# Optimization experiments

Hardware: AMD Instinct MI355X
Metric: run time of the kernel (lower is better)

The kernel has to match this reference:

```python
import jax, jax.numpy as jnp
import numpy as np

B, N_ATOM, N_TOK = 1, 1536, 384
C_ATOM, C_PAIR, C_TOK = 128, 16, 384
C_HID, H, L = 32, 4, 3
HID = 2 * C_ATOM  # n_transition = 2
N_QUERY, N_KEY, INF = 32, 128, 1e9


def _ln(x, gamma=None, beta=None, eps=1e-5):
    mu = jnp.mean(x, axis=-1, keepdims=True)
    var = jnp.mean(jnp.square(x - mu), axis=-1, keepdims=True)
    y = (x - mu) * jax.lax.rsqrt(var + eps)
    if gamma is not None:
        y = y * gamma
    if beta is not None:
        y = y + beta
    return y


def _adaln(a, s, gamma_s, Wg, bg, Ws):
    an = _ln(a)            # LN without affine
    sn = _ln(s, gamma_s)   # scale-only LN
    return jax.nn.sigmoid(sn @ Wg + bg) * an + sn @ Ws


def _block_mask():
    # AtomTransformer.forward: 32-query x 128-key block-local mask
    offset = N_QUERY // 2 - 0.5
    n_center = N_ATOM // N_QUERY + 1
    centers = offset + jnp.arange(n_center, dtype=jnp.float32) * N_QUERY
    idx = jnp.arange(N_ATOM, dtype=jnp.float32)[:, None]
    row = (jnp.abs(idx - centers[None, :]) < N_QUERY / 2).astype(jnp.float32)
    col = (jnp.abs(idx - centers[None, :]) < N_KEY / 2).astype(jnp.float32)
    return (row @ col.T - 1.0) * INF   # [N,N]: 0 in-window, -INF outside


def _forward(ref_pos, ref_mask, ref_element, ref_charge, ref_atom_name_chars,
             ref_space_uid, token_mask, atom_to_token_index,
             W_feats, W_ref_offset, W_inv_sq, W_valid, W_l, W_m,
             W_mlp1, W_mlp2, W_mlp3, W_out_tok,
             attn_ada_gamma_s, attn_ada_Wg, attn_ada_bg, attn_ada_Ws,
             Wq, bq, Wk, Wv, lnz_g, lnz_b, Wb, Wgate, Wo, Wsg, bsg,
             tr_ada_gamma_s, tr_ada_Wg, tr_ada_bg, tr_ada_Ws,
             tr_W1, tr_W2, tr_Wog, tr_bog, tr_Wout):
    # --- RefAtomFeatureEmbedder (AF3 Alg 5 lines 1-6) ---
    feats = jnp.concatenate([
        ref_pos, ref_mask[..., None], ref_element, ref_charge[..., None],
        ref_atom_name_chars.reshape(B, N_ATOM, -1), ref_space_uid[..., None]], axis=-1)
    cl = feats @ W_feats                                     # [B,N,C_ATOM]
    d = ref_pos[:, None, :, :] - ref_pos[:, :, None, :]      # d[l,m] = pos[m]-pos[l]
    v = (ref_space_uid[:, None, :] == ref_space_uid[:, :, None]).astype(jnp.float32)[..., None]
    plm = (d @ W_ref_offset) * v
    inv_sq = 1.0 / (1.0 + jnp.sum(d * d, axis=-1, keepdims=True))
    plm = plm + (inv_sq @ W_inv_sq) * v + (v @ W_valid) * v  # [B,N,N,C_PAIR]
    ql = cl
    # --- single -> pair conditioning + pair MLP ---
    crelu = jax.nn.relu(cl)
    plm = plm + (crelu @ W_l)[:, :, None, :] + (crelu @ W_m)[:, None, :, :]
    h = jax.nn.relu(plm) @ W_mlp1
    h = jax.nn.relu(h) @ W_mlp2
    h = jax.nn.relu(h) @ W_mlp3
    plm = plm + h
    # --- AtomTransformer (Alg 7) -> DiffusionTransformer (Alg 23) ---
    beta = _block_mask()                                     # [N,N]
    atom_mask = jnp.einsum('blt,bt->bl', atom_to_token_index, token_mask)
    mask_bias = (atom_mask - 1.0)[:, None, None, :] * INF    # [B,1,1,N]
    a, s = ql, cl
    inv_sqrt = 1.0 / np.sqrt(C_HID)
    for i in range(L):
        # AttentionPairBias (Alg 24)
        an = _adaln(a, s, attn_ada_gamma_s[i], attn_ada_Wg[i], attn_ada_bg[i], attn_ada_Ws[i])
        q = (an @ Wq[i] + bq[i]).reshape(B, N_ATOM, H, C_HID)
        k = (an @ Wk[i]).reshape(B, N_ATOM, H, C_HID)
        vv = (an @ Wv[i]).reshape(B, N_ATOM, H, C_HID)
        zb = _ln(plm, lnz_g[i], lnz_b[i]) @ Wb[i]            # [B,N,N,H]
        logits = (jnp.einsum('bqhc,bkhc->bhqk', q, k) * inv_sqrt
                  + jnp.moveaxis(zb, -1, 1) + beta[None, None] + mask_bias)
        A = jax.nn.softmax(logits, axis=-1)
        o = jnp.einsum('bhqk,bkhc->bqhc', A, vv)
        g = jax.nn.sigmoid(an @ Wgate[i]).reshape(B, N_ATOM, H, C_HID)
        o = (g * o).reshape(B, N_ATOM, H * C_HID) @ Wo[i]
        attn_out = jax.nn.sigmoid(s @ Wsg[i] + bsg[i]) * o
        # ConditionedTransitionBlock (Alg 25) on pre-attention a (Alg 23)
        tn = _adaln(a, s, tr_ada_gamma_s[i], tr_ada_Wg[i], tr_ada_bg[i], tr_ada_Ws[i])
        hh = jax.nn.silu(tn @ tr_W1[i]) * (tn @ tr_W2[i])
        tr_out = jax.nn.sigmoid(s @ tr_Wog[i] + tr_bog[i]) * (hh @ tr_Wout[i])
        a = attn_out + tr_out
    # --- mean-aggregate atoms -> tokens (Alg 5 line 15) ---
    al = jax.nn.relu(a @ W_out_tok)                          # [B,N,C_TOK]
    counts = jnp.maximum(jnp.sum(atom_to_token_index, axis=1), 1.0)
    a_tok = jnp.einsum('blt,blc->btc', atom_to_token_index, al) / counts[..., None]
    return a_tok


def setup_inputs() -> dict:
    key = jax.random.key(0)
    ks = iter(jax.random.split(key, 80))

    def nrm(shape, scale=0.02):
        return jax.random.normal(next(ks), shape, dtype=jnp.float32) * scale

    inp = {}
    inp['ref_pos'] = jax.random.normal(next(ks), (B, N_ATOM, 3), dtype=jnp.float32) * 3.0
    inp['ref_mask'] = jnp.ones((B, N_ATOM), jnp.float32)
    elem = jax.random.randint(next(ks), (B, N_ATOM), 0, 128)
    inp['ref_element'] = jax.nn.one_hot(elem, 128, dtype=jnp.float32)
    inp['ref_charge'] = jax.random.normal(next(ks), (B, N_ATOM), dtype=jnp.float32)
    chars = jax.random.randint(next(ks), (B, N_ATOM, 4), 0, 64)
    inp['ref_atom_name_chars'] = jax.nn.one_hot(chars, 64, dtype=jnp.float32)
    inp['ref_space_uid'] = jnp.broadcast_to(
        (jnp.arange(N_ATOM) // 8).astype(jnp.float32), (B, N_ATOM))
    inp['token_mask'] = jnp.ones((B, N_TOK), jnp.float32)
    tok = (jnp.arange(N_ATOM) * N_TOK) // N_ATOM  # ~4 atoms per token
    inp['atom_to_token_index'] = jnp.broadcast_to(
        jax.nn.one_hot(tok, N_TOK, dtype=jnp.float32), (B, N_ATOM, N_TOK))
    # embedder params
    inp['W_feats'] = nrm((390, C_ATOM))
    inp['W_ref_offset'] = nrm((3, C_PAIR))
    inp['W_inv_sq'] = nrm((1, C_PAIR))
    inp['W_valid'] = nrm((1, C_PAIR))
    inp['W_l'] = nrm((C_ATOM, C_PAIR))
    inp['W_m'] = nrm((C_ATOM, C_PAIR))
    inp['W_mlp1'] = nrm((C_PAIR, C_PAIR))
    inp['W_mlp2'] = nrm((C_PAIR, C_PAIR))
    inp['W_mlp3'] = nrm((C_PAIR, C_PAIR))
    inp['W_out_tok'] = nrm((C_ATOM, C_TOK))
    # DiffusionTransformer params, stacked over L blocks
    inp['attn_ada_gamma_s'] = jnp.ones((L, C_ATOM), jnp.float32)
    inp['attn_ada_Wg'] = nrm((L, C_ATOM, C_ATOM))
    inp['attn_ada_bg'] = jnp.zeros((L, C_ATOM), jnp.float32)
    inp['attn_ada_Ws'] = nrm((L, C_ATOM, C_ATOM))
    inp['Wq'] = nrm((L, C_ATOM, H * C_HID))
    inp['bq'] = jnp.zeros((L, H * C_HID), jnp.float32)
    inp['Wk'] = nrm((L, C_ATOM, H * C_HID))
    inp['Wv'] = nrm((L, C_ATOM, H * C_HID))
    inp['lnz_g'] = jnp.ones((L, C_PAIR), jnp.float32)
    inp['lnz_b'] = jnp.zeros((L, C_PAIR), jnp.float32)
    inp['Wb'] = nrm((L, C_PAIR, H))
    inp['Wgate'] = nrm((L, C_ATOM, H * C_HID))
    inp['Wo'] = nrm((L, H * C_HID, C_ATOM))
    inp['Wsg'] = nrm((L, C_ATOM, C_ATOM))
    inp['bsg'] = jnp.full((L, C_ATOM), -2.0, jnp.float32)
    inp['tr_ada_gamma_s'] = jnp.ones((L, C_ATOM), jnp.float32)
    inp['tr_ada_Wg'] = nrm((L, C_ATOM, C_ATOM))
    inp['tr_ada_bg'] = jnp.zeros((L, C_ATOM), jnp.float32)
    inp['tr_ada_Ws'] = nrm((L, C_ATOM, C_ATOM))
    inp['tr_W1'] = nrm((L, C_ATOM, HID))
    inp['tr_W2'] = nrm((L, C_ATOM, HID))
    inp['tr_Wog'] = nrm((L, C_ATOM, C_ATOM))
    inp['tr_bog'] = jnp.full((L, C_ATOM), -2.0, jnp.float32)
    inp['tr_Wout'] = nrm((L, HID, C_ATOM))
    return inp


def reference(ref_pos, ref_mask, ref_element, ref_charge, ref_atom_name_chars,
              ref_space_uid, token_mask, atom_to_token_index,
              W_feats, W_ref_offset, W_inv_sq, W_valid, W_l, W_m,
              W_mlp1, W_mlp2, W_mlp3, W_out_tok,
              attn_ada_gamma_s, attn_ada_Wg, attn_ada_bg, attn_ada_Ws,
              Wq, bq, Wk, Wv, lnz_g, lnz_b, Wb, Wgate, Wo, Wsg, bsg,
              tr_ada_gamma_s, tr_ada_Wg, tr_ada_bg, tr_ada_Ws,
              tr_W1, tr_W2, tr_Wog, tr_bog, tr_Wout):
    return _forward(ref_pos, ref_mask, ref_element, ref_charge, ref_atom_name_chars,
                    ref_space_uid, token_mask, atom_to_token_index,
                    W_feats, W_ref_offset, W_inv_sq, W_valid, W_l, W_m,
                    W_mlp1, W_mlp2, W_mlp3, W_out_tok,
                    attn_ada_gamma_s, attn_ada_Wg, attn_ada_bg, attn_ada_Ws,
                    Wq, bq, Wk, Wv, lnz_g, lnz_b, Wb, Wgate, Wo, Wsg, bsg,
                    tr_ada_gamma_s, tr_ada_Wg, tr_ada_bg, tr_ada_Ws,
                    tr_W1, tr_W2, tr_Wog, tr_bog, tr_Wout)
```

## Files before the change

kernel.cpp:

```cpp
#include <hip/hip_runtime.h>
#include <math.h>

#define N_ATOM 1536
#define NLAYER 3
#define NC     196608L
#define ZSTRIDE 786432L

struct GD { const float* A; const float* B; float* C; const float* ks; const float* bias;
            const float* sg; const float* ad; int act; int ldb; int ldc; int mode; };
struct GB { GD g[18]; };

__global__ __launch_bounds__(128) void embed_tok_kernel(
    const float* __restrict__ pos, const float* __restrict__ rmask,
    const float* __restrict__ elem, const float* __restrict__ charge,
    const float* __restrict__ chars, const float* __restrict__ uid,
    const float* __restrict__ Wf, const float* __restrict__ W_l, const float* __restrict__ W_m,
    const float* __restrict__ a2t, const float* __restrict__ tmask,
    float* __restrict__ cl, float* __restrict__ aa,
    float* __restrict__ pl, float* __restrict__ pm,
    int* __restrict__ tok, float* __restrict__ amask)
{
  int l = blockIdx.x, c = threadIdx.x;
  __shared__ int sidx[6];
  __shared__ float crow[128];
  if (elem[(long)l * 128 + c] > 0.5f) sidx[0] = c;
  float v0 = chars[(long)l * 256 + c];
  if (v0 > 0.5f) sidx[1 + (c >> 6)] = c & 63;
  float v1 = chars[(long)l * 256 + 128 + c];
  if (v1 > 0.5f) sidx[3 + (c >> 6)] = c & 63;
  for (int j = c; j < 384; j += 128)
    if (a2t[(long)l * 384 + j] > 0.5f) sidx[5] = j;
  __syncthreads();
  float acc = pos[l * 3 + 0] * Wf[c]
            + pos[l * 3 + 1] * Wf[128 + c]
            + pos[l * 3 + 2] * Wf[256 + c]
            + rmask[l] * Wf[384 + c]
            + Wf[(4 + sidx[0]) * 128 + c]
            + charge[l] * Wf[132 * 128 + c]
            + Wf[(133 + sidx[1]) * 128 + c]
            + Wf[(197 + sidx[2]) * 128 + c]
            + Wf[(261 + sidx[3]) * 128 + c]
            + Wf[(325 + sidx[4]) * 128 + c]
            + uid[l] * Wf[389 * 128 + c];
  long gi = (long)l * 128 + c;
  cl[gi] = acc; aa[gi] = acc; crow[c] = fmaxf(acc, 0.f);
  __syncthreads();
  if (c < 32) {
    const float* W = (c < 16) ? W_l : W_m;
    int o = c & 15;
    float s = 0.f;
    for (int cc = 0; cc < 128; cc++) s = fmaf(crow[cc], W[cc * 16 + o], s);
    if (c < 16) pl[l * 16 + o] = s; else pm[l * 16 + o] = s;
  }
  if (c == 127) {
    int j = sidx[5];
    tok[l] = j; amask[l] = tmask[j];
  }
}

__device__ __forceinline__ void gemm32_body(float* sm, const GD d, int row0, int col0) {
  float* As = sm;
  float* Bs = sm + 1152;
  float* rmu = sm + 3328;
  float* rsd = sm + 3360;
  int tid = threadIdx.x;
  if (d.mode >= 1) {
    int r = tid >> 3, sgi = tid & 7;
    const float* Ar = d.A + (long)(row0 + r) * 128 + sgi * 16;
    float4 vv[4];
    float s1 = 0.f;
#pragma unroll
    for (int c4 = 0; c4 < 4; c4++) {
      vv[c4] = *(const float4*)(Ar + c4 * 4);
      s1 += vv[c4].x + vv[c4].y + vv[c4].z + vv[c4].w;
    }
    s1 += __shfl_xor(s1, 1); s1 += __shfl_xor(s1, 2); s1 += __shfl_xor(s1, 4);
    float mu = s1 * (1.f / 128.f);
    float s2 = 0.f;
#pragma unroll
    for (int c4 = 0; c4 < 4; c4++) {
      float dx = vv[c4].x - mu, dy = vv[c4].y - mu, dz = vv[c4].z - mu, dw = vv[c4].w - mu;
      s2 += dx * dx + dy * dy + dz * dz + dw * dw;
    }
    s2 += __shfl_xor(s2, 1); s2 += __shfl_xor(s2, 2); s2 += __shfl_xor(s2, 4);
    if (sgi == 0) {
      rmu[r] = mu;
      rsd[r] = rsqrtf(s2 * (1.f / 128.f) + 1e-5f);
    }
  }
  int tx = tid & 15, ty = tid >> 4;
  float acc[2][4] = {};
  for (int k0 = 0; k0 < 128; k0 += 32) {
    __syncthreads();
    { int r = tid >> 3, k4 = tid & 7;
      long gro = (long)(row0 + r) * 128 + k0 + k4 * 4;
      float4 v = *(const float4*)(d.A + gro);
      float vals[4] = {v.x, v.y, v.z, v.w};
      if (d.mode >= 1) {
        float mu = rmu[r], sd = rsd[r];
        if (d.mode == 2) {
          float4 sg4 = *(const float4*)(d.sg + gro);
          float4 ad4 = *(const float4*)(d.ad + gro);
          vals[0] = fmaf(sg4.x, (vals[0] - mu) * sd, ad4.x);
          vals[1] = fmaf(sg4.y, (vals[1] - mu) * sd, ad4.y);
          vals[2] = fmaf(sg4.z, (vals[2] - mu) * sd, ad4.z);
          vals[3] = fmaf(sg4.w, (vals[3] - mu) * sd, ad4.w);
        } else {
#pragma unroll
          for (int cc = 0; cc < 4; cc++) vals[cc] = (vals[cc] - mu) * sd;
        }
      }
      if (d.ks) {
        const float* kp = d.ks + k0 + k4 * 4;
#pragma unroll
        for (int cc = 0; cc < 4; cc++) vals[cc] *= kp[cc];
      }
      As[(k4 * 4 + 0) * 36 + r] = vals[0]; As[(k4 * 4 + 1) * 36 + r] = vals[1];
      As[(k4 * 4 + 2) * 36 + r] = vals[2]; As[(k4 * 4 + 3) * 36 + r] = vals[3];
    }
    for (int e = tid; e < 512; e += 256) {
      int k = e >> 4, n4 = e & 15;
      *(float4*)&Bs[k * 68 + n4 * 4] = *(const float4*)(d.B + (long)(k0 + k) * d.ldb + col0 + n4 * 4);
    }
    __syncthreads();
#pragma unroll
    for (int kk = 0; kk < 32; kk++) {
      float a0 = As[kk * 36 + ty * 2], a1 = As[kk * 36 + ty * 2 + 1];
      float4 b = *(const float4*)&Bs[kk * 68 + tx * 4];
      float bv[4] = {b.x, b.y, b.z, b.w};
#pragma unroll
      for (int j = 0; j < 4; j++) {
        acc[0][j] = fmaf(a0, bv[j], acc[0][j]);
        acc[1][j] = fmaf(a1, bv[j], acc[1][j]);
      }
    }
  }
#pragma unroll
  for (int i = 0; i < 2; i++) {
    int row = row0 + ty * 2 + i;
#pragma unroll
    for (int j = 0; j < 4; j++) {
      int col = col0 + tx * 4 + j;
      float x = acc[i][j];
      if (d.bias) x += d.bias[col];
      if (d.act == 1) x = 1.f / (1.f + expf(-x));
      else if (d.act == 2) x = fmaxf(x, 0.f);
      d.C[(long)row * d.ldc + col] = x;
    }
  }
}

__device__ __forceinline__ void gemm32k64_body(float* sm, const GD d, int row0, int col0) {
  float* As = sm;
  float* Bs = sm + 2304;
  float* rmu = sm + 6656;
  float* rsd = sm + 6688;
  int tid = threadIdx.x;
  if (d.mode >= 1) {
    int r = tid >> 3, sgi = tid & 7;
    const float* Ar = d.A + (long)(row0 + r) * 128 + sgi * 16;
    float4 vv[4];
    float s1 = 0.f;
#pragma unroll
    for (int c4 = 0; c4 < 4; c4++) {
      vv[c4] = *(const float4*)(Ar + c4 * 4);
      s1 += vv[c4].x + vv[c4].y + vv[c4].z + vv[c4].w;
    }
    s1 += __shfl_xor(s1, 1); s1 += __shfl_xor(s1, 2); s1 += __shfl_xor(s1, 4);
    float mu = s1 * (1.f / 128.f);
    float s2 = 0.f;
#pragma unroll
    for (int c4 = 0; c4 < 4; c4++) {
      float dx = vv[c4].x - mu, dy = vv[c4].y - mu, dz = vv[c4].z - mu, dw = vv[c4].w - mu;
      s2 += dx * dx + dy * dy + dz * dz + dw * dw;
    }
    s2 += __shfl_xor(s2, 1); s2 += __shfl_xor(s2, 2); s2 += __shfl_xor(s2, 4);
    if (sgi == 0) {
      rmu[r] = mu;
      rsd[r] = rsqrtf(s2 * (1.f / 128.f) + 1e-5f);
    }
  }
  int tx = tid & 15, ty = tid >> 4;
  float acc[2][4] = {};
  for (int k0 = 0; k0 < 128; k0 += 64) {
    __syncthreads();
    { int r = tid >> 3, k4b = tid & 7;
#pragma unroll
      for (int kh = 0; kh < 2; kh++) {
        int k4 = k4b + kh * 8;
        long gro = (long)(row0 + r) * 128 + k0 + k4 * 4;
        float4 v = *(const float4*)(d.A + gro);
        float vals[4] = {v.x, v.y, v.z, v.w};
        if (d.mode >= 1) {
          float mu = rmu[r], sd = rsd[r];
          if (d.mode == 2) {
            float4 sg4 = *(const float4*)(d.sg + gro);
            float4 ad4 = *(const float4*)(d.ad + gro);
            vals[0] = fmaf(sg4.x, (vals[0] - mu) * sd, ad4.x);
            vals[1] = fmaf(sg4.y, (vals[1] - mu) * sd, ad4.y);
            vals[2] = fmaf(sg4.z, (vals[2] - mu) * sd, ad4.z);
            vals[3] = fmaf(sg4.w, (vals[3] - mu) * sd, ad4.w);
          } else {
#pragma unroll
            for (int cc = 0; cc < 4; cc++) vals[cc] = (vals[cc] - mu) * sd;
          }
        }
        if (d.ks) {
          const float* kp = d.ks + k0 + k4 * 4;
#pragma unroll
          for (int cc = 0; cc < 4; cc++) vals[cc] *= kp[cc];
        }
        As[(k4 * 4 + 0) * 36 + r] = vals[0]; As[(k4 * 4 + 1) * 36 + r] = vals[1];
        As[(k4 * 4 + 2) * 36 + r] = vals[2]; As[(k4 * 4 + 3) * 36 + r] = vals[3];
      } }
    for (int e = tid; e < 1024; e += 256) {
      int k = e >> 4, n4 = e & 15;
      *(float4*)&Bs[k * 68 + n4 * 4] = *(const float4*)(d.B + (long)(k0 + k) * d.ldb + col0 + n4 * 4);
    }
    __syncthreads();
#pragma unroll
    for (int kk = 0; kk < 64; kk++) {
      float a0 = As[kk * 36 + ty * 2], a1 = As[kk * 36 + ty * 2 + 1];
      float4 b = *(const float4*)&Bs[kk * 68 + tx * 4];
      float bv[4] = {b.x, b.y, b.z, b.w};
#pragma unroll
      for (int j = 0; j < 4; j++) {
        acc[0][j] = fmaf(a0, bv[j], acc[0][j]);
        acc[1][j] = fmaf(a1, bv[j], acc[1][j]);
      }
    }
  }
#pragma unroll
  for (int i = 0; i < 2; i++) {
    int row = row0 + ty * 2 + i;
#pragma unroll
    for (int j = 0; j < 4; j++) {
      int col = col0 + tx * 4 + j;
      float x = acc[i][j];
      if (d.bias) x += d.bias[col];
      if (d.act == 1) x = 1.f / (1.f + expf(-x));
      else if (d.act == 2) x = fmaxf(x, 0.f);
      d.C[(long)row * d.ldc + col] = x;
    }
  }
}

__global__ __launch_bounds__(256) void gemm32(GB args)
{
  __shared__ __align__(16) float sm[6720];
  gemm32k64_body(sm, args.g[blockIdx.z], blockIdx.y * 32, blockIdx.x * 64);
}

__global__ __launch_bounds__(256) void zpre_kernel(
    const float* __restrict__ pos, const float* __restrict__ uid,
    const float* __restrict__ Wro, const float* __restrict__ Winv, const float* __restrict__ Wval,
    const float* __restrict__ M1, const float* __restrict__ M2, const float* __restrict__ M3,
    const float* __restrict__ Lg, const float* __restrict__ Lb, const float* __restrict__ Wb,
    const float* __restrict__ pl, const float* __restrict__ pm, float* __restrict__ zb,
    GB ba)
{
  __shared__ __align__(16) float sm[3392];
  int bid = blockIdx.x, tid = threadIdx.x;
  if (bid < 1728) {
    GD d = ba.g[bid / 96];
    int tt = bid % 96;
    gemm32_body(sm, d, (tt >> 1) * 32, (tt & 1) * 64);
    return;
  }
  int zbid = bid - 1728;
  if (tid < 48)  sm[tid] = Wro[tid];
  if (tid < 16)  { sm[48 + tid] = Winv[tid]; sm[64 + tid] = Wval[tid]; }
  sm[80 + tid] = M1[tid]; sm[336 + tid] = M2[tid]; sm[592 + tid] = M3[tid];
  if (tid < 48)  { sm[848 + tid] = Lg[tid]; sm[896 + tid] = Lb[tid]; }
  if (tid < 192) sm[944 + tid] = Wb[tid];
  __syncthreads();
  const float* sWro = sm;      const float* sWinv = sm + 48;  const float* sWval = sm + 64;
  const float* sM1 = sm + 80;  const float* sM2 = sm + 336;   const float* sM3 = sm + 592;
  const float* sLg = sm + 848; const float* sLb = sm + 896;   const float* sWb = sm + 944;
  int b = zbid >> 4;
  int pc = (zbid & 15) * 256 + tid;
  int qi = pc >> 7, kj = pc & 127;
  int l = b * 32 + qi, m = b * 32 - 48 + kj;
  long base = (long)(b * 32 + qi) * 128 + kj;
  if (m < 0 || m >= N_ATOM) {
    for (int i = 0; i < NLAYER; i++)
      for (int h = 0; h < 4; h++) zb[i * ZSTRIDE + h * NC + base] = 0.f;
    return;
  }
  float dx = pos[m * 3 + 0] - pos[l * 3 + 0];
  float dy = pos[m * 3 + 1] - pos[l * 3 + 1];
  float dz = pos[m * 3 + 2] - pos[l * 3 + 2];
  float v = (uid[m] == uid[l]) ? 1.f : 0.f;
  float inv = 1.f / (1.f + dx * dx + dy * dy + dz * dz);
  float pv[16], ha[16], hb[16];
#pragma unroll
  for (int j = 0; j < 16; j++)
    pv[j] = v * (dx * sWro[j] + dy * sWro[16 + j] + dz * sWro[32 + j] + inv * sWinv[j] + sWval[j])
            + pl[l * 16 + j] + pm[m * 16 + j];
#pragma unroll
  for (int jo = 0; jo < 16; jo++) { float s = 0.f; for (int ji = 0; ji < 16; ji++) s = fmaf(fmaxf(pv[ji], 0.f), sM1[ji * 16 + jo], s); ha[jo] = s; }
#pragma unroll
  for (int jo = 0; jo < 16; jo++) { float s = 0.f; for (int ji = 0; ji < 16; ji++) s = fmaf(fmaxf(ha[ji], 0.f), sM2[ji * 16 + jo], s); hb[jo] = s; }
#pragma unroll
  for (int jo = 0; jo < 16; jo++) { float s = 0.f; for (int ji = 0; ji < 16; ji++) s = fmaf(fmaxf(hb[ji], 0.f), sM3[ji * 16 + jo], s); ha[jo] = s; }
#pragma unroll
  for (int j = 0; j < 16; j++) pv[j] += ha[j];
  for (int i = 0; i < NLAYER; i++) {
    float mu = 0.f;
#pragma unroll
    for (int j = 0; j < 16; j++) mu += pv[j];
    mu *= (1.f / 16.f);
    float var = 0.f;
#pragma unroll
    for (int j = 0; j < 16; j++) { float dd = pv[j] - mu; var += dd * dd; }
    var *= (1.f / 16.f);
    float rs = rsqrtf(var + 1e-5f);
    float zn[16];
#pragma unroll
    for (int j = 0; j < 16; j++) zn[j] = (pv[j] - mu) * rs * sLg[i * 16 + j] + sLb[i * 16 + j];
    for (int h = 0; h < 4; h++) {
      float s = 0.f;
#pragma unroll
      for (int j = 0; j < 16; j++) s = fmaf(zn[j], sWb[i * 64 + j * 4 + h], s);
      zb[i * ZSTRIDE + h * NC + base] = s;
    }
  }
}

__global__ __launch_bounds__(256) void attn_tr_kernel(
    const float* __restrict__ qb, const float* __restrict__ kb, const float* __restrict__ vb,
    const float* __restrict__ gb, const float* __restrict__ zb, const float* __restrict__ amask,
    float* __restrict__ go,
    const float* __restrict__ h1, const float* __restrict__ h2, const float* __restrict__ B2,
    const float* __restrict__ g2, float* __restrict__ trbuf)
{
  __shared__ __align__(16) float sm[11904];
  int bid = blockIdx.x, t = threadIdx.x;
  if (bid < 96) {
    int u = bid;
    int row0 = (u >> 1) * 32, col0 = (u & 1) * 64;
    float* As = sm; float* Bs = sm + 2304;
    int tx = t & 15, ty = t >> 4;
    float acc2[2][4] = {};
    for (int k0 = 0; k0 < 256; k0 += 64) {
      __syncthreads();
      { int r = t >> 3, k4b = t & 7;
#pragma unroll
        for (int kh = 0; kh < 2; kh++) {
          int k4 = k4b + kh * 8;
          long o = (long)(row0 + r) * 256 + k0 + k4 * 4;
          float4 x = *(const float4*)(h1 + o);
          float4 y = *(const float4*)(h2 + o);
          As[(k4 * 4 + 0) * 36 + r] = (x.x / (1.f + expf(-x.x))) * y.x;
          As[(k4 * 4 + 1) * 36 + r] = (x.y / (1.f + expf(-x.y))) * y.y;
          As[(k4 * 4 + 2) * 36 + r] = (x.z / (1.f + expf(-x.z))) * y.z;
          As[(k4 * 4 + 3) * 36 + r] = (x.w / (1.f + expf(-x.w))) * y.w;
        } }
      for (int e = t; e < 1024; e += 256) {
        int k = e >> 4, n4 = e & 15;
        *(float4*)&Bs[k * 68 + n4 * 4] = *(const float4*)(B2 + (long)(k0 + k) * 128 + col0 + n4 * 4);
      }
      __syncthreads();
#pragma unroll
      for (int kk = 0; kk < 64; kk++) {
        float a0 = As[kk * 36 + ty * 2], a1 = As[kk * 36 + ty * 2 + 1];
        float4 b = *(const float4*)&Bs[kk * 68 + tx * 4];
        float bv[4] = {b.x, b.y, b.z, b.w};
#pragma unroll
        for (int j = 0; j < 4; j++) {
          acc2[0][j] = fmaf(a0, bv[j], acc2[0][j]);
          acc2[1][j] = fmaf(a1, bv[j], acc2[1][j]);
        }
      }
    }
#pragma unroll
    for (int i = 0; i < 2; i++) {
      long o = (long)(row0 + ty * 2 + i) * 128 + col0 + tx * 4;
      float4 g4 = *(const float4*)(g2 + o);
      float4 r;
      r.x = g4.x * acc2[i][0]; r.y = g4.y * acc2[i][1];
      r.z = g4.z * acc2[i][2]; r.w = g4.w * acc2[i][3];
      *(float4*)(trbuf + o) = r;
    }
    return;
  }
  float* qs = sm;
  float* ks = sm + 576;
  float* vs = sm + 5184;
  float* ps = sm + 9792;
  int u = bid - 96;
  int h = u / 96, bx = u - h * 96;
  int b = bx >> 1, half = bx & 1;
  int q0 = b * 32 + half * 16;
  int kbase = b * 32 - 48;
  const float* zbh = zb + (long)h * NC;
  if (t < 128) {
    int qi = t >> 3, c4 = t & 7;
    *(float4*)&qs[qi * 36 + c4 * 4] = *(const float4*)(qb + (long)(q0 + qi) * 128 + h * 32 + c4 * 4);
  }
  for (int idx = t; idx < 128 * 8; idx += 256) {
    int kj = idx >> 3, c4 = idx & 7;
    int m = kbase + kj;
    float4 kv = make_float4(0.f, 0.f, 0.f, 0.f), vv = make_float4(0.f, 0.f, 0.f, 0.f);
    if (m >= 0 && m < N_ATOM) {
      kv = *(const float4*)(kb + (long)m * 128 + h * 32 + c4 * 4);
      vv = *(const float4*)(vb + (long)m * 128 + h * 32 + c4 * 4);
    }
    *(float4*)&ks[kj * 36 + c4 * 4] = kv;
    *(float4*)&vs[kj * 36 + c4 * 4] = vv;
  }
  __syncthreads();
  const float isq = 0.17677669529663687f;
  for (int p = t; p < 2048; p += 256) {
    int qi = p >> 7, kj = p & 127;
    int m = kbase + kj;
    float s = 0.f;
#pragma unroll
    for (int c4 = 0; c4 < 8; c4++) {
      float4 a = *(const float4*)&qs[qi * 36 + c4 * 4];
      float4 k4 = *(const float4*)&ks[kj * 36 + c4 * 4];
      s = fmaf(a.x, k4.x, s); s = fmaf(a.y, k4.y, s);
      s = fmaf(a.z, k4.z, s); s = fmaf(a.w, k4.w, s);
    }
    float logit;
    if (m >= 0 && m < N_ATOM) {
      logit = s * isq + zbh[(long)(q0 + qi) * 128 + kj] + (amask[m] - 1.f) * 1e9f;
    } else {
      logit = -1e9f;
    }
    ps[qi * 132 + kj] = logit;
  }
  __syncthreads();
  {
    int row = t >> 4, ln = t & 15;
    float mx = -1e30f;
    for (int kj = ln; kj < 128; kj += 16) mx = fmaxf(mx, ps[row * 132 + kj]);
#pragma unroll
    for (int o = 8; o > 0; o >>= 1) mx = fmaxf(mx, __shfl_xor(mx, o));
    float smv = 0.f;
    for (int kj = ln; kj < 128; kj += 16) { float e = expf(ps[row * 132 + kj] - mx); ps[row * 132 + kj] = e; smv += e; }
#pragma unroll
    for (int o = 8; o > 0; o >>= 1) smv += __shfl_xor(smv, o);
    float r = 1.f / smv;
    for (int kj = ln; kj < 128; kj += 16) ps[row * 132 + kj] *= r;
  }
  __syncthreads();
  {
    int qi = t >> 4, seg = (t >> 3) & 1, c4 = t & 7;
    float4 acc = make_float4(0.f, 0.f, 0.f, 0.f);
    int kj0 = seg * 64;
#pragma unroll 4
    for (int kj = kj0; kj < kj0 + 64; kj++) {
      float p = ps[qi * 132 + kj];
      float4 v = *(const float4*)&vs[kj * 36 + c4 * 4];
      acc.x = fmaf(p, v.x, acc.x); acc.y = fmaf(p, v.y, acc.y);
      acc.z = fmaf(p, v.z, acc.z); acc.w = fmaf(p, v.w, acc.w);
    }
    acc.x += __shfl_xor(acc.x, 8);
    acc.y += __shfl_xor(acc.y, 8);
    acc.z += __shfl_xor(acc.z, 8);
    acc.w += __shfl_xor(acc.w, 8);
    if (seg == 0) {
      long gi = (long)(q0 + qi) * 128 + h * 32 + c4 * 4;
      float4 g = *(const float4*)(gb + gi);
      acc.x *= g.x; acc.y *= g.y; acc.z *= g.z; acc.w *= g.w;
      *(float4*)(go + gi) = acc;
    }
  }
}

__global__ __launch_bounds__(256) void wo_kernel(
    const float* __restrict__ A1, const float* __restrict__ B1,
    const float* __restrict__ g1, const float* __restrict__ tr,
    float* __restrict__ C)
{
  __shared__ __align__(16) float As[64 * 36];
  __shared__ __align__(16) float Bs[64 * 68];
  const int N = 128;
  int t = threadIdx.x;
  int row0 = blockIdx.y * 32, col0 = blockIdx.x * 64;
  int tx = t & 15, ty = t >> 4;
  float acc1[2][4] = {};
  for (int k0 = 0; k0 < 128; k0 += 64) {
    __syncthreads();
    { int r = t >> 3, k4b = t & 7;
#pragma unroll
      for (int kh = 0; kh < 2; kh++) {
        int k4 = k4b + kh * 8;
        float4 v = *(const float4*)(A1 + (long)(row0 + r) * 128 + k0 + k4 * 4);
        As[(k4 * 4 + 0) * 36 + r] = v.x; As[(k4 * 4 + 1) * 36 + r] = v.y;
        As[(k4 * 4 + 2) * 36 + r] = v.z; As[(k4 * 4 + 3) * 36 + r] = v.w;
      } }
    for (int e = t; e < 1024; e += 256) {
      int k = e >> 4, n4 = e & 15;
      *(float4*)&Bs[k * 68 + n4 * 4] = *(const float4*)(B1 + (long)(k0 + k) * N + col0 + n4 * 4);
    }
    __syncthreads();
#pragma unroll
    for (int kk = 0; kk < 64; kk++) {
      float a0 = As[kk * 36 + ty * 2], a1 = As[kk * 36 + ty * 2 + 1];
      float4 b = *(const float4*)&Bs[kk * 68 + tx * 4];
      float bv[4] = {b.x, b.y, b.z, b.w};
#pragma unroll
      for (int j = 0; j < 4; j++) {
        acc1[0][j] = fmaf(a0, bv[j], acc1[0][j]);
        acc1[1][j] = fmaf(a1, bv[j], acc1[1][j]);
      }
    }
  }
#pragma unroll
  for (int i = 0; i < 2; i++) {
    long o = (long)(row0 + ty * 2 + i) * N + col0 + tx * 4;
    float4 ga = *(const float4*)(g1 + o);
    float4 tv = *(const float4*)(tr + o);
    float4 r;
    r.x = ga.x * acc1[i][0] + tv.x;
    r.y = ga.y * acc1[i][1] + tv.y;
    r.z = ga.z * acc1[i][2] + tv.z;
    r.w = ga.w * acc1[i][3] + tv.w;
    *(float4*)(C + o) = r;
  }
}

__global__ __launch_bounds__(256) void gemm_scatter(
    const float* __restrict__ A, const float* __restrict__ B,
    const int* __restrict__ tok,
    float* __restrict__ out, int K)
{
  __shared__ __align__(16) float As[32][68];
  __shared__ __align__(16) float Bs[32][68];
  int tid = threadIdx.x;
  int row0 = blockIdx.y * 64, col0 = blockIdx.x * 64;
  int tx = tid & 15, ty = tid >> 4;
  float acc[4][4] = {};
  for (int k0 = 0; k0 < K; k0 += 32) {
    __syncthreads();
    { int r = tid >> 3, k4 = tid & 7;
#pragma unroll
      for (int half = 0; half < 2; half++) {
        int row = r + half * 32;
        float4 v = *(const float4*)(A + (long)(row0 + row) * K + k0 + k4 * 4);
        As[k4 * 4 + 0][row] = v.x; As[k4 * 4 + 1][row] = v.y;
        As[k4 * 4 + 2][row] = v.z; As[k4 * 4 + 3][row] = v.w;
      } }
    { int kk = tid >> 4, n4 = tid & 15;
#pragma unroll
      for (int half = 0; half < 2; half++) {
        int k = kk + half * 16;
        float4 v = *(const float4*)(B + (long)(k0 + k) * 384 + col0 + n4 * 4);
        *(float4*)&Bs[k][n4 * 4] = v;
      } }
    __syncthreads();
#pragma unroll
    for (int kk = 0; kk < 32; kk++) {
      float4 a = *(const float4*)&As[kk][ty * 4];
      float4 b = *(const float4*)&Bs[kk][tx * 4];
      float av[4] = {a.x, a.y, a.z, a.w}, bv[4] = {b.x, b.y, b.z, b.w};
#pragma unroll
      for (int i = 0; i < 4; i++)
#pragma unroll
        for (int j = 0; j < 4; j++) acc[i][j] = fmaf(av[i], bv[j], acc[i][j]);
    }
  }
  __syncthreads();
  int r0 = row0 + ty * 4;
  int t0 = tok[r0];
  int cnt = 0;
#pragma unroll
  for (int i = 0; i < 4; i++) cnt += (tok[r0 + i] == t0) ? 1 : 0;
  float inv = 1.f / fmaxf((float)cnt, 1.f);
#pragma unroll
  for (int j = 0; j < 4; j++) {
    int col = col0 + tx * 4 + j;
    float s = 0.f;
#pragma unroll
    for (int i = 0; i < 4; i++)
      if (tok[r0 + i] == t0) s += fmaxf(acc[i][j], 0.f);
    out[(long)t0 * 384 + col] = s * inv;
  }
}

extern "C" void kernel_launch(void* const* d_in, const int* in_sizes, int n_in,
                              void* d_out, int out_size, void* d_ws, size_t ws_size,
                              hipStream_t stream)
{
  const float* pos    = (const float*)d_in[0];
  const float* rmask  = (const float*)d_in[1];
  const float* elem   = (const float*)d_in[2];
  const float* charge = (const float*)d_in[3];
  const float* chars  = (const float*)d_in[4];
  const float* uid    = (const float*)d_in[5];
  const float* tmask  = (const float*)d_in[6];
  const float* a2t    = (const float*)d_in[7];
  const float* Wf     = (const float*)d_in[8];
  const float* Wro    = (const float*)d_in[9];
  const float* Winv   = (const float*)d_in[10];
  const float* Wval   = (const float*)d_in[11];
  const float* W_l    = (const float*)d_in[12];
  const float* W_m    = (const float*)d_in[13];
  const float* M1     = (const float*)d_in[14];
  const float* M2     = (const float*)d_in[15];
  const float* M3     = (const float*)d_in[16];
  const float* Wtok   = (const float*)d_in[17];
  const float* gA     = (const float*)d_in[18];
  const float* WgA    = (const float*)d_in[19];
  const float* bgA    = (const float*)d_in[20];
  const float* WsA    = (const float*)d_in[21];
  const float* Wq     = (const float*)d_in[22];
  const float* bq     = (const float*)d_in[23];
  const float* Wk     = (const float*)d_in[24];
  const float* Wv     = (const float*)d_in[25];
  const float* Lg     = (const float*)d_in[26];
  const float* Lb     = (const float*)d_in[27];
  const float* Wb     = (const float*)d_in[28];
  const float* Wgate  = (const float*)d_in[29];
  const float* Wo     = (const float*)d_in[30];
  const float* Wsg    = (const float*)d_in[31];
  const float* bsg    = (const float*)d_in[32];
  const float* gT     = (const float*)d_in[33];
  const float* WgT    = (const float*)d_in[34];
  const float* bgT    = (const float*)d_in[35];
  const float* WsT    = (const float*)d_in[36];
  const float* trW1   = (const float*)d_in[37];
  const float* trW2   = (const float*)d_in[38];
  const float* Wog    = (const float*)d_in[39];
  const float* bog    = (const float*)d_in[40];
  const float* Wout   = (const float*)d_in[41];
  float* out = (float*)d_out;

  float* ws = (float*)d_ws;
  size_t off = 0;
  auto alloc = [&](size_t n) { float* p = ws + off; off += n; return p; };
  float* cl     = alloc(NC);
  float* aa     = alloc(NC);
  float* qbuf   = alloc(NC);
  float* kbuf   = alloc(NC);
  float* vbuf   = alloc(NC);
  float* gbuf   = alloc(NC);
  float* gobuf  = alloc(NC);
  float* trbuf  = alloc(NC);
  float* h1     = alloc((size_t)N_ATOM * 256);
  float* h2     = alloc((size_t)N_ATOM * 256);
  float* pl     = alloc((size_t)N_ATOM * 16);
  float* pm     = alloc((size_t)N_ATOM * 16);
  float* zbias  = alloc((size_t)NLAYER * ZSTRIDE);
  float* sgA    = alloc(NC * NLAYER);
  float* adA    = alloc(NC * NLAYER);
  float* sgT    = alloc(NC * NLAYER);
  float* adT    = alloc(NC * NLAYER);
  float* gsg    = alloc(NC * NLAYER);
  float* gog    = alloc(NC * NLAYER);
  float* amask  = alloc(N_ATOM);
  int*   tok    = (int*)alloc(N_ATOM);
  (void)ws_size; (void)in_sizes; (void)n_in; (void)out_size;

  embed_tok_kernel<<<N_ATOM, 128, 0, stream>>>(pos, rmask, elem, charge, chars, uid, Wf,
                                               W_l, W_m, a2t, tmask,
                                               cl, aa, pl, pm, tok, amask);

  {
    GB ba = {};
    for (int i = 0; i < NLAYER; i++) {
      size_t o = (size_t)i * NC;
      ba.g[i * 6 + 0] = { cl, WgA + i * 16384, sgA + o, gA + i * 128, bgA + i * 128, nullptr, nullptr, 1, 128, 128, 1 };
      ba.g[i * 6 + 1] = { cl, WsA + i * 16384, adA + o, gA + i * 128, nullptr,       nullptr, nullptr, 0, 128, 128, 1 };
      ba.g[i * 6 + 2] = { cl, WgT + i * 16384, sgT + o, gT + i * 128, bgT + i * 128, nullptr, nullptr, 1, 128, 128, 1 };
      ba.g[i * 6 + 3] = { cl, WsT + i * 16384, adT + o, gT + i * 128, nullptr,       nullptr, nullptr, 0, 128, 128, 1 };
      ba.g[i * 6 + 4] = { cl, Wsg + i * 16384, gsg + o, nullptr,      bsg + i * 128, nullptr, nullptr, 1, 128, 128, 0 };
      ba.g[i * 6 + 5] = { cl, Wog + i * 16384, gog + o, nullptr,      bog + i * 128, nullptr, nullptr, 1, 128, 128, 0 };
    }
    zpre_kernel<<<1728 + 768, 256, 0, stream>>>(pos, uid, Wro, Winv, Wval, M1, M2, M3,
                                                Lg, Lb, Wb, pl, pm, zbias, ba);
  }

  for (int i = 0; i < NLAYER; i++) {
    size_t o = (size_t)i * NC;
    {
      GB ba = {};
      ba.g[0] = { aa, Wq + i * 16384,        qbuf,     nullptr, bq + i * 128, sgA + o, adA + o, 0, 128, 128, 2 };
      ba.g[1] = { aa, Wk + i * 16384,        kbuf,     nullptr, nullptr,      sgA + o, adA + o, 0, 128, 128, 2 };
      ba.g[2] = { aa, Wv + i * 16384,        vbuf,     nullptr, nullptr,      sgA + o, adA + o, 0, 128, 128, 2 };
      ba.g[3] = { aa, Wgate + i * 16384,     gbuf,     nullptr, nullptr,      sgA + o, adA + o, 1, 128, 128, 2 };
      ba.g[4] = { aa, trW1 + i * 32768,       h1,      nullptr, nullptr,      sgT + o, adT + o, 0, 256, 256, 2 };
      ba.g[5] = { aa, trW1 + i * 32768 + 128, h1 + 128, nullptr, nullptr,     sgT + o, adT + o, 0, 256, 256, 2 };
      ba.g[6] = { aa, trW2 + i * 32768,       h2,      nullptr, nullptr,      sgT + o, adT + o, 0, 256, 256, 2 };
      ba.g[7] = { aa, trW2 + i * 32768 + 128, h2 + 128, nullptr, nullptr,     sgT + o, adT + o, 0, 256, 256, 2 };
      gemm32<<<dim3(2, 48, 8), 256, 0, stream>>>(ba);
    }
    attn_tr_kernel<<<480, 256, 0, stream>>>(qbuf, kbuf, vbuf, gbuf,
                                            zbias + (size_t)i * ZSTRIDE, amask, gobuf,
                                            h1, h2, Wout + i * 32768, gog + o, trbuf);
    wo_kernel<<<dim3(2, 48), 256, 0, stream>>>(gobuf, Wo + i * 16384, gsg + o, trbuf, aa);
  }

  gemm_scatter<<<dim3(6, 24), 256, 0, stream>>>(aa, Wtok, tok, out, 128);
}
```

Before: 302.7 us.

## Fuse output projection into next layer's projection GEMM and final scatter

```diff
diff --git a/kernel.cpp b/kernel.cpp
--- a/kernel.cpp
+++ b/kernel.cpp
@@ -7,7 +7,8 @@
 #define ZSTRIDE 786432L
 
 struct GD { const float* A; const float* B; float* C; const float* ks; const float* bias;
-            const float* sg; const float* ad; int act; int ldb; int ldc; int mode; };
+            const float* sg; const float* ad; const float* Wp; const float* g1; const float* t2;
+            int act; int ldb; int ldc; int mode; };
 struct GB { GD g[18]; };
 
 __global__ __launch_bounds__(128) void embed_tok_kernel(
@@ -150,17 +151,57 @@
   }
 }
 
-__device__ __forceinline__ void gemm32k64_body(float* sm, const GD d, int row0, int col0) {
-  float* As = sm;
-  float* Bs = sm + 2304;
-  float* rmu = sm + 6656;
-  float* rsd = sm + 6688;
+__device__ __forceinline__ void gemm32c_body(float* sm, const GD d, int row0, int col0) {
+  float* As = sm; float* Bs = sm + 1152;
+  float* rmu = sm + 3328; float* rsd = sm + 3360;
+  float* Aeff = sm + 3392;
   int tid = threadIdx.x;
-  if (d.mode >= 1) {
-    int r = tid >> 3, sgi = tid & 7;
-    const float* Ar = d.A + (long)(row0 + r) * 128 + sgi * 16;
-    float4 vv[4];
-    float s1 = 0.f;
+  int tx = tid & 15, ty = tid >> 4;
+#pragma unroll
+  for (int ch = 0; ch < 2; ch++) {
+    int cc0 = ch * 64;
+    float acc[2][4] = {};
+    for (int k0 = 0; k0 < 128; k0 += 32) {
+      __syncthreads();
+      { int r = tid >> 3, k4 = tid & 7;
+        long gro = (long)(row0 + r) * 128 + k0 + k4 * 4;
+        float4 v = *(const float4*)(d.A + gro);
+        As[(k4 * 4 + 0) * 36 + r] = v.x; As[(k4 * 4 + 1) * 36 + r] = v.y;
+        As[(k4 * 4 + 2) * 36 + r] = v.z; As[(k4 * 4 + 3) * 36 + r] = v.w;
+      }
+      for (int e = tid; e < 512; e += 256) {
+        int k = e >> 4, n4 = e & 15;
+        *(float4*)&Bs[k * 68 + n4 * 4] = *(const float4*)(d.Wp + (long)(k0 + k) * 128 + cc0 + n4 * 4);
+      }
+      __syncthreads();
+#pragma unroll
+      for (int kk = 0; kk < 32; kk++) {
+        float a0 = As[kk * 36 + ty * 2], a1 = As[kk * 36 + ty * 2 + 1];
+        float4 b = *(const float4*)&Bs[kk * 68 + tx * 4];
+        float bv[4] = {b.x, b.y, b.z, b.w};
+#pragma unroll
+        for (int j = 0; j < 4; j++) {
+          acc[0][j] = fmaf(a0, bv[j], acc[0][j]);
+          acc[1][j] = fmaf(a1, bv[j], acc[1][j]);
+        }
+      }
+    }
+#pragma unroll
+    for (int i = 0; i < 2; i++) {
+      long go_ = (long)(row0 + ty * 2 + i) * 128 + cc0 + tx * 4;
+      float4 ga = *(const float4*)(d.g1 + go_);
+      float4 tv = *(const float4*)(d.t2 + go_);
+      float* ae = &Aeff[(ty * 2 + i) * 132 + cc0 + tx * 4];
+      ae[0] = fmaf(ga.x, acc[i][0], tv.x);
+      ae[1] = fmaf(ga.y, acc[i][1], tv.y);
+      ae[2] = fmaf(ga.z, acc[i][2], tv.z);
+      ae[3] = fmaf(ga.w, acc[i][3], tv.w);
+    }
+  }
+  __syncthreads();
+  { int r = tid >> 3, sgi = tid & 7;
+    const float* Ar = Aeff + r * 132 + sgi * 16;
+    float4 vv[4]; float s1 = 0.f;
 #pragma unroll
     for (int c4 = 0; c4 < 4; c4++) {
       vv[c4] = *(const float4*)(Ar + c4 * 4);
@@ -175,51 +216,29 @@
       s2 += dx * dx + dy * dy + dz * dz + dw * dw;
     }
     s2 += __shfl_xor(s2, 1); s2 += __shfl_xor(s2, 2); s2 += __shfl_xor(s2, 4);
-    if (sgi == 0) {
-      rmu[r] = mu;
-      rsd[r] = rsqrtf(s2 * (1.f / 128.f) + 1e-5f);
-    }
-  }
-  int tx = tid & 15, ty = tid >> 4;
+    if (sgi == 0) { rmu[r] = mu; rsd[r] = rsqrtf(s2 * (1.f / 128.f) + 1e-5f); }
+  }
   float acc[2][4] = {};
-  for (int k0 = 0; k0 < 128; k0 += 64) {
+  for (int k0 = 0; k0 < 128; k0 += 32) {
     __syncthreads();
-    { int r = tid >> 3, k4b = tid & 7;
-#pragma unroll
-      for (int kh = 0; kh < 2; kh++) {
-        int k4 = k4b + kh * 8;
-        long gro = (long)(row0 + r) * 128 + k0 + k4 * 4;
-        float4 v = *(const float4*)(d.A + gro);
-        float vals[4] = {v.x, v.y, v.z, v.w};
-        if (d.mode >= 1) {
-          float mu = rmu[r], sd = rsd[r];
-          if (d.mode == 2) {
-            float4 sg4 = *(const float4*)(d.sg + gro);
-            float4 ad4 = *(const float4*)(d.ad + gro);
-            vals[0] = fmaf(sg4.x, (vals[0] - mu) * sd, ad4.x);
-            vals[1] = fmaf(sg4.y, (vals[1] - mu) * sd, ad4.y);
-            vals[2] = fmaf(sg4.z, (vals[2] - mu) * sd, ad4.z);
-            vals[3] = fmaf(sg4.w, (vals[3] - mu) * sd, ad4.w);
-          } else {
-#pragma unroll
-            for (int cc = 0; cc < 4; cc++) vals[cc] = (vals[cc] - mu) * sd;
-          }
-        }
-        if (d.ks) {
-          const float* kp = d.ks + k0 + k4 * 4;
-#pragma unroll
-          for (int cc = 0; cc < 4; cc++) vals[cc] *= kp[cc];
-        }
-        As[(k4 * 4 + 0) * 36 + r] = vals[0]; As[(k4 * 4 + 1) * 36 + r] = vals[1];
-        As[(k4 * 4 + 2) * 36 + r] = vals[2]; As[(k4 * 4 + 3) * 36 + r] = vals[3];
-      } }
-    for (int e = tid; e < 1024; e += 256) {
+    { int r = tid >> 3, k4 = tid & 7;
+      long gro = (long)(row0 + r) * 128 + k0 + k4 * 4;
+      float4 v = *(const float4*)&Aeff[r * 132 + k0 + k4 * 4];
+      float mu = rmu[r], sd = rsd[r];
+      float4 sg4 = *(const float4*)(d.sg + gro);
+      float4 ad4 = *(const float4*)(d.ad + gro);
+      As[(k4 * 4 + 0) * 36 + r] = fmaf(sg4.x, (v.x - mu) * sd, ad4.x);
+      As[(k4 * 4 + 1) * 36 + r] = fmaf(sg4.y, (v.y - mu) * sd, ad4.y);
+      As[(k4 * 4 + 2) * 36 + r] = fmaf(sg4.z, (v.z - mu) * sd, ad4.z);
+      As[(k4 * 4 + 3) * 36 + r] = fmaf(sg4.w, (v.w - mu) * sd, ad4.w);
+    }
+    for (int e = tid; e < 512; e += 256) {
       int k = e >> 4, n4 = e & 15;
       *(float4*)&Bs[k * 68 + n4 * 4] = *(const float4*)(d.B + (long)(k0 + k) * d.ldb + col0 + n4 * 4);
     }
     __syncthreads();
 #pragma unroll
-    for (int kk = 0; kk < 64; kk++) {
+    for (int kk = 0; kk < 32; kk++) {
       float a0 = As[kk * 36 + ty * 2], a1 = As[kk * 36 + ty * 2 + 1];
       float4 b = *(const float4*)&Bs[kk * 68 + tx * 4];
       float bv[4] = {b.x, b.y, b.z, b.w};
@@ -247,8 +266,10 @@
 
 __global__ __launch_bounds__(256) void gemm32(GB args)
 {
-  __shared__ __align__(16) float sm[6720];
-  gemm32k64_body(sm, args.g[blockIdx.z], blockIdx.y * 32, blockIdx.x * 64);
+  __shared__ __align__(16) float sm[7616];
+  GD d = args.g[blockIdx.z];
+  if (d.mode == 3) gemm32c_body(sm, d, blockIdx.y * 32, blockIdx.x * 64);
+  else             gemm32_body(sm, d, blockIdx.y * 32, blockIdx.x * 64);
 }
 
 __global__ __launch_bounds__(256) void zpre_kernel(
@@ -469,92 +490,88 @@
   }
 }
 
-__global__ __launch_bounds__(256) void wo_kernel(
-    const float* __restrict__ A1, const float* __restrict__ B1,
-    const float* __restrict__ g1, const float* __restrict__ tr,
-    float* __restrict__ C)
+__global__ __launch_bounds__(256) void gemm_scatter(
+    const float* __restrict__ G, const float* __restrict__ Wp,
+    const float* __restrict__ g1, const float* __restrict__ t2,
+    const float* __restrict__ B,
+    const int* __restrict__ tok,
+    float* __restrict__ out)
 {
-  __shared__ __align__(16) float As[64 * 36];
-  __shared__ __align__(16) float Bs[64 * 68];
-  const int N = 128;
-  int t = threadIdx.x;
-  int row0 = blockIdx.y * 32, col0 = blockIdx.x * 64;
-  int tx = t & 15, ty = t >> 4;
-  float acc1[2][4] = {};
-  for (int k0 = 0; k0 < 128; k0 += 64) {
-    __syncthreads();
-    { int r = t >> 3, k4b = t & 7;
-#pragma unroll
-      for (int kh = 0; kh < 2; kh++) {
-        int k4 = k4b + kh * 8;
-        float4 v = *(const float4*)(A1 + (long)(row0 + r) * 128 + k0 + k4 * 4);
-        As[(k4 * 4 + 0) * 36 + r] = v.x; As[(k4 * 4 + 1) * 36 + r] = v.y;
-        As[(k4 * 4 + 2) * 36 + r] = v.z; As[(k4 * 4 + 3) * 36 + r] = v.w;
-      } }
-    for (int e = t; e < 1024; e += 256) {
-      int k = e >> 4, n4 = e & 15;
-      *(float4*)&Bs[k * 68 + n4 * 4] = *(const float4*)(B1 + (long)(k0 + k) * N + col0 + n4 * 4);
-    }
-    __syncthreads();
-#pragma unroll
-    for (int kk = 0; kk < 64; kk++) {
-      float a0 = As[kk * 36 + ty * 2], a1 = As[kk * 36 + ty * 2 + 1];
-      float4 b = *(const float4*)&Bs[kk * 68 + tx * 4];
-      float bv[4] = {b.x, b.y, b.z, b.w};
-#pragma unroll
-      for (int j = 0; j < 4; j++) {
-        acc1[0][j] = fmaf(a0, bv[j], acc1[0][j]);
-        acc1[1][j] = fmaf(a1, bv[j], acc1[1][j]);
-      }
-    }
-  }
-#pragma unroll
-  for (int i = 0; i < 2; i++) {
-    long o = (long)(row0 + ty * 2 + i) * N + col0 + tx * 4;
-    float4 ga = *(const float4*)(g1 + o);
-    float4 tv = *(const float4*)(tr + o);
-    float4 r;
-    r.x = ga.x * acc1[i][0] + tv.x;
-    r.y = ga.y * acc1[i][1] + tv.y;
-    r.z = ga.z * acc1[i][2] + tv.z;
-    r.w = ga.w * acc1[i][3] + tv.w;
-    *(float4*)(C + o) = r;
-  }
-}
-
-__global__ __launch_bounds__(256) void gemm_scatter(
-    const float* __restrict__ A, const float* __restrict__ B,
-    const int* __restrict__ tok,
-    float* __restrict__ out, int K)
-{
-  __shared__ __align__(16) float As[32][68];
-  __shared__ __align__(16) float Bs[32][68];
+  __shared__ __align__(16) float sm[12800];
+  float* As = sm;
+  float* Bs = sm + 2176;
+  float* Aeff = sm + 4352;
   int tid = threadIdx.x;
   int row0 = blockIdx.y * 64, col0 = blockIdx.x * 64;
   int tx = tid & 15, ty = tid >> 4;
+#pragma unroll
+  for (int rh = 0; rh < 2; rh++) {
+    int rr0 = row0 + rh * 32;
+#pragma unroll
+    for (int ch = 0; ch < 2; ch++) {
+      int cc0 = ch * 64;
+      float acc[2][4] = {};
+      for (int k0 = 0; k0 < 128; k0 += 32) {
+        __syncthreads();
+        { int r = tid >> 3, k4 = tid & 7;
+          long gro = (long)(rr0 + r) * 128 + k0 + k4 * 4;
+          float4 v = *(const float4*)(G + gro);
+          As[(k4 * 4 + 0) * 68 + r] = v.x; As[(k4 * 4 + 1) * 68 + r] = v.y;
+          As[(k4 * 4 + 2) * 68 + r] = v.z; As[(k4 * 4 + 3) * 68 + r] = v.w;
+        }
+        for (int e = tid; e < 512; e += 256) {
+          int k = e >> 4, n4 = e & 15;
+          *(float4*)&Bs[k * 68 + n4 * 4] = *(const float4*)(Wp + (long)(k0 + k) * 128 + cc0 + n4 * 4);
+        }
+        __syncthreads();
+#pragma unroll
+        for (int kk = 0; kk < 32; kk++) {
+          float a0 = As[kk * 68 + ty * 2], a1 = As[kk * 68 + ty * 2 + 1];
+          float4 b = *(const float4*)&Bs[kk * 68 + tx * 4];
+          float bv[4] = {b.x, b.y, b.z, b.w};
+#pragma unroll
+          for (int j = 0; j < 4; j++) {
+            acc[0][j] = fmaf(a0, bv[j], acc[0][j]);
+            acc[1][j] = fmaf(a1, bv[j], acc[1][j]);
+          }
+        }
+      }
+#pragma unroll
+      for (int i = 0; i < 2; i++) {
+        long go_ = (long)(rr0 + ty * 2 + i) * 128 + cc0 + tx * 4;
+        float4 ga = *(const float4*)(g1 + go_);
+        float4 tv = *(const float4*)(t2 + go_);
+        float* ae = &Aeff[(rh * 32 + ty * 2 + i) * 132 + cc0 + tx * 4];
+        ae[0] = fmaf(ga.x, acc[i][0], tv.x);
+        ae[1] = fmaf(ga.y, acc[i][1], tv.y);
+        ae[2] = fmaf(ga.z, acc[i][2], tv.z);
+        ae[3] = fmaf(ga.w, acc[i][3], tv.w);
+      }
+    }
+  }
+  __syncthreads();
   float acc[4][4] = {};
-  for (int k0 = 0; k0 < K; k0 += 32) {
+  for (int k0 = 0; k0 < 128; k0 += 32) {
     __syncthreads();
     { int r = tid >> 3, k4 = tid & 7;
 #pragma unroll
       for (int half = 0; half < 2; half++) {
         int row = r + half * 32;
-        float4 v = *(const float4*)(A + (long)(row0 + row) * K + k0 + k4 * 4);
-        As[k4 * 4 + 0][row] = v.x; As[k4 * 4 + 1][row] = v.y;
-        As[k4 * 4 + 2][row] = v.z; As[k4 * 4 + 3][row] = v.w;
+        float4 v = *(const float4*)&Aeff[row * 132 + k0 + k4 * 4];
+        As[(k4 * 4 + 0) * 68 + row] = v.x; As[(k4 * 4 + 1) * 68 + row] = v.y;
+        As[(k4 * 4 + 2) * 68 + row] = v.z; As[(k4 * 4 + 3) * 68 + row] = v.w;
       } }
     { int kk = tid >> 4, n4 = tid & 15;
 #pragma unroll
       for (int half = 0; half < 2; half++) {
         int k = kk + half * 16;
-        float4 v = *(const float4*)(B + (long)(k0 + k) * 384 + col0 + n4 * 4);
-        *(float4*)&Bs[k][n4 * 4] = v;
+        *(float4*)&Bs[k * 68 + n4 * 4] = *(const float4*)(B + (long)(k0 + k) * 384 + col0 + n4 * 4);
       } }
     __syncthreads();
 #pragma unroll
     for (int kk = 0; kk < 32; kk++) {
-      float4 a = *(const float4*)&As[kk][ty * 4];
-      float4 b = *(const float4*)&Bs[kk][tx * 4];
+      float4 a = *(const float4*)&As[kk * 68 + ty * 4];
+      float4 b = *(const float4*)&Bs[kk * 68 + tx * 4];
       float av[4] = {a.x, a.y, a.z, a.w}, bv[4] = {b.x, b.y, b.z, b.w};
 #pragma unroll
       for (int i = 0; i < 4; i++)
@@ -662,12 +679,12 @@
     GB ba = {};
     for (int i = 0; i < NLAYER; i++) {
       size_t o = (size_t)i * NC;
-      ba.g[i * 6 + 0] = { cl, WgA + i * 16384, sgA + o, gA + i * 128, bgA + i * 128, nullptr, nullptr, 1, 128, 128, 1 };
-      ba.g[i * 6 + 1] = { cl, WsA + i * 16384, adA + o, gA + i * 128, nullptr,       nullptr, nullptr, 0, 128, 128, 1 };
-      ba.g[i * 6 + 2] = { cl, WgT + i * 16384, sgT + o, gT + i * 128, bgT + i * 128, nullptr, nullptr, 1, 128, 128, 1 };
-      ba.g[i * 6 + 3] = { cl, WsT + i * 16384, adT + o, gT + i * 128, nullptr,       nullptr, nullptr, 0, 128, 128, 1 };
-      ba.g[i * 6 + 4] = { cl, Wsg + i * 16384, gsg + o, nullptr,      bsg + i * 128, nullptr, nullptr, 1, 128, 128, 0 };
-      ba.g[i * 6 + 5] = { cl, Wog + i * 16384, gog + o, nullptr,      bog + i * 128, nullptr, nullptr, 1, 128, 128, 0 };
+      ba.g[i * 6 + 0] = { cl, WgA + i * 16384, sgA + o, gA + i * 128, bgA + i * 128, nullptr, nullptr, nullptr, nullptr, nullptr, 1, 128, 128, 1 };
+      ba.g[i * 6 + 1] = { cl, WsA + i * 16384, adA + o, gA + i * 128, nullptr,       nullptr, nullptr, nullptr, nullptr, nullptr, 0, 128, 128, 1 };
+      ba.g[i * 6 + 2] = { cl, WgT + i * 16384, sgT + o, gT + i * 128, bgT + i * 128, nullptr, nullptr, nullptr, nullptr, nullptr, 1, 128, 128, 1 };
+      ba.g[i * 6 + 3] = { cl, WsT + i * 16384, adT + o, gT + i * 128, nullptr,       nullptr, nullptr, nullptr, nullptr, nullptr, 0, 128, 128, 1 };
+      ba.g[i * 6 + 4] = { cl, Wsg + i * 16384, gsg + o, nullptr,      bsg + i * 128, nullptr, nullptr, nullptr, nullptr, nullptr, 1, 128, 128, 0 };
+      ba.g[i * 6 + 5] = { cl, Wog + i * 16384, gog + o, nullptr,      bog + i * 128, nullptr, nullptr, nullptr, nullptr, nullptr, 1, 128, 128, 0 };
     }
     zpre_kernel<<<1728 + 768, 256, 0, stream>>>(pos, uid, Wro, Winv, Wval, M1, M2, M3,
                                                 Lg, Lb, Wb, pl, pm, zbias, ba);
@@ -677,21 +694,36 @@
     size_t o = (size_t)i * NC;
     {
       GB ba = {};
-      ba.g[0] = { aa, Wq + i * 16384,        qbuf,     nullptr, bq + i * 128, sgA + o, adA + o, 0, 128, 128, 2 };
-      ba.g[1] = { aa, Wk + i * 16384,        kbuf,     nullptr, nullptr,      sgA + o, adA + o, 0, 128, 128, 2 };
-      ba.g[2] = { aa, Wv + i * 16384,        vbuf,     nullptr, nullptr,      sgA + o, adA + o, 0, 128, 128, 2 };
-      ba.g[3] = { aa, Wgate + i * 16384,     gbuf,     nullptr, nullptr,      sgA + o, adA + o, 1, 128, 128, 2 };
-      ba.g[4] = { aa, trW1 + i * 32768,       h1,      nullptr, nullptr,      sgT + o, adT + o, 0, 256, 256, 2 };
-      ba.g[5] = { aa, trW1 + i * 32768 + 128, h1 + 128, nullptr, nullptr,     sgT + o, adT + o, 0, 256, 256, 2 };
-      ba.g[6] = { aa, trW2 + i * 32768,       h2,      nullptr, nullptr,      sgT + o, adT + o, 0, 256, 256, 2 };
-      ba.g[7] = { aa, trW2 + i * 32768 + 128, h2 + 128, nullptr, nullptr,     sgT + o, adT + o, 0, 256, 256, 2 };
+      for (int s = 0; s < 8; s++) {
+        GD& d = ba.g[s];
+        d.ks = nullptr; d.bias = nullptr; d.act = 0;
+        if (i == 0) {
+          d.A = aa; d.Wp = nullptr; d.g1 = nullptr; d.t2 = nullptr; d.mode = 2;
+        } else {
+          d.A = gobuf; d.Wp = Wo + (i - 1) * 16384;
+          d.g1 = gsg + (size_t)(i - 1) * NC; d.t2 = trbuf; d.mode = 3;
+        }
+        if (s < 4) { d.sg = sgA + o; d.ad = adA + o; d.ldb = 128; d.ldc = 128; }
+        else       { d.sg = sgT + o; d.ad = adT + o; d.ldb = 256; d.ldc = 256; }
+        switch (s) {
+          case 0: d.B = Wq + i * 16384;          d.C = qbuf;     d.bias = bq + i * 128; break;
+          case 1: d.B = Wk + i * 16384;          d.C = kbuf;     break;
+          case 2: d.B = Wv + i * 16384;          d.C = vbuf;     break;
+          case 3: d.B = Wgate + i * 16384;       d.C = gbuf;     d.act = 1; break;
+          case 4: d.B = trW1 + i * 32768;        d.C = h1;       break;
+          case 5: d.B = trW1 + i * 32768 + 128;  d.C = h1 + 128; break;
+          case 6: d.B = trW2 + i * 32768;        d.C = h2;       break;
+          default:d.B = trW2 + i * 32768 + 128;  d.C = h2 + 128; break;
+        }
+      }
       gemm32<<<dim3(2, 48, 8), 256, 0, stream>>>(ba);
     }
     attn_tr_kernel<<<480, 256, 0, stream>>>(qbuf, kbuf, vbuf, gbuf,
                                             zbias + (size_t)i * ZSTRIDE, amask, gobuf,
                                             h1, h2, Wout + i * 32768, gog + o, trbuf);
-    wo_kernel<<<dim3(2, 48), 256, 0, stream>>>(gobuf, Wo + i * 16384, gsg + o, trbuf, aa);
-  }
-
-  gemm_scatter<<<dim3(6, 24), 256, 0, stream>>>(aa, Wtok, tok, out, 128);
+  }
+
+  gemm_scatter<<<dim3(6, 24), 256, 0, stream>>>(gobuf, Wo + 2 * 16384,
+                                                gsg + (size_t)2 * NC, trbuf,
+                                                Wtok, tok, out);
 }
```

Measured after the change: 333.8 us. 10.3% more time.
